# Performance work log

Measured on AMD Instinct MI355X. Metric: run time of the kernel, lower is better.

Reference implementation:

```python
import jax, jax.numpy as jnp
import numpy as np

K = 5        # kernel_size per pseudo-dim
DIM = 2      # pseudo-coordinate dimensionality
K2 = K * K   # total kernel weight matrices
N_NODES = 50000


def spline_basis(edge_attr):
    """Open B-spline basis, degree=1, dim=2. Returns basis [E,4], weight_index [E,4]."""
    v = edge_attr * (K - 1)                      # [E,2], pseudo in [0,1]
    lo = jnp.floor(v)
    frac = v - lo                                # [E,2]
    lo = lo.astype(jnp.int32)
    fac = jnp.stack([1.0 - frac, frac], axis=-1)                 # [E,2,2] (dim, bit)
    idx = jnp.clip(lo[..., None] + jnp.arange(2), 0, K - 1)      # [E,2,2]
    b0 = jnp.array([0, 1, 0, 1])  # bit for dim 0, per spline term
    b1 = jnp.array([0, 0, 1, 1])  # bit for dim 1
    basis = fac[:, 0, b0] * fac[:, 1, b1]        # [E,4]
    wi = idx[:, 0, b0] * K + idx[:, 1, b1]       # [E,4] flat kernel index
    return basis, wi


def spline_conv(x, src, dst, basis, wi, W, root, bias, n_nodes):
    """SplineConv with mean aggregation, root weight and bias.
    x:[N,Fin] W:[K2,Fin,Fout] root:[Fin,Fout] bias:[Fout]"""
    E = src.shape[0]
    K2_, Fin, Fout = W.shape
    # scatter the 4 sparse basis values into a dense per-edge kernel-coeff matrix [E,K2]
    coeff = jnp.zeros((E, K2_), x.dtype).at[jnp.arange(E)[:, None], wi].add(basis)
    xj = x[src]                                  # gather source features [E,Fin]
    msg = jnp.zeros((E, Fout), x.dtype)
    for k in range(K2_):                         # fixed small loop over 25 kernels
        msg = msg + coeff[:, k:k + 1] * (xj @ W[k])
    agg = jax.ops.segment_sum(msg, dst, num_segments=n_nodes)    # [N,Fout]
    deg = jax.ops.segment_sum(jnp.ones((E,), x.dtype), dst, num_segments=n_nodes)
    agg = agg / jnp.clip(deg, 1.0)[:, None]      # mean aggregation
    return agg + x @ root + bias


def setup_inputs() -> dict:
    key = jax.random.key(0)
    ks = jax.random.split(key, 9)
    E = 800000
    Fin, H, C = 64, 16, 7
    x = jax.random.normal(ks[0], (N_NODES, Fin), dtype=jnp.float32)
    edge_index = jax.random.randint(ks[1], (2, E), 0, N_NODES, dtype=jnp.int64)
    edge_attr = jax.random.uniform(ks[2], (E, DIM), dtype=jnp.float32)
    s1 = 1.0 / np.sqrt(Fin)
    s2 = 1.0 / np.sqrt(H)
    W1 = jax.random.uniform(ks[3], (K2, Fin, H), jnp.float32, -s1, s1)
    root1 = jax.random.uniform(ks[4], (Fin, H), jnp.float32, -s1, s1)
    bias1 = jax.random.uniform(ks[5], (H,), jnp.float32, -s1, s1)
    W2 = jax.random.uniform(ks[6], (K2, H, C), jnp.float32, -s2, s2)
    root2 = jax.random.uniform(ks[7], (H, C), jnp.float32, -s2, s2)
    bias2 = jax.random.uniform(ks[8], (C,), jnp.float32, -s2, s2)
    return {"x": x, "edge_index": edge_index, "edge_attr": edge_attr,
            "W1": W1, "root1": root1, "bias1": bias1,
            "W2": W2, "root2": root2, "bias2": bias2}


def reference(x, edge_index, edge_attr, W1, root1, bias1, W2, root2, bias2):
    src = edge_index[0]
    dst = edge_index[1]
    basis, wi = spline_basis(edge_attr)
    h = jax.nn.relu(spline_conv(x, src, dst, basis, wi, W1, root1, bias1, N_NODES))
    # dropout(p=0.6) is identity in eval mode
    out = spline_conv(h, src, dst, basis, wi, W2, root2, bias2, N_NODES)
    return jax.nn.log_softmax(out, axis=1)
```

## Files before the change

### kernel.cpp

```cpp
#include <hip/hip_runtime.h>

#define KK2 25
#define FIN 64
#define HH 16
#define CC 7

#define SCAN_VPT 4
#define SCAN_BLK 256
#define SCAN_CHUNK (SCAN_VPT * SCAN_BLK)

__global__ void k_hist(const int* __restrict__ ei, int* __restrict__ cnt, int E) {
    int e = blockIdx.x * 256 + threadIdx.x;
    if (e < E) atomicAdd(&cnt[ei[E + e]], 1);
}

__global__ void k_bsum(const int* __restrict__ cnt, int* __restrict__ bsum, int N) {
    int b = blockIdx.x, t = threadIdx.x;
    int base = b * SCAN_CHUNK + t * SCAN_VPT;
    int s = 0;
#pragma unroll
    for (int j = 0; j < SCAN_VPT; j++) {
        int i = base + j;
        if (i < N) s += cnt[i];
    }
#pragma unroll
    for (int d = 1; d < 64; d <<= 1) s += __shfl_xor(s, d, 64);
    __shared__ int sd[SCAN_BLK / 64];
    if ((t & 63) == 0) sd[t >> 6] = s;
    __syncthreads();
    if (t == 0) {
        int tot = 0;
        for (int w = 0; w < SCAN_BLK / 64; w++) tot += sd[w];
        bsum[b] = tot;
    }
}

__global__ void k_bscan(const int* __restrict__ bsum, int* __restrict__ boff, int nblk) {
    int t = threadIdx.x;
    __shared__ int sd[256];
    int v = (t < nblk) ? bsum[t] : 0;
    sd[t] = v;
    __syncthreads();
    for (int off = 1; off < 256; off <<= 1) {
        int u = (t >= off) ? sd[t - off] : 0;
        __syncthreads();
        sd[t] += u;
        __syncthreads();
    }
    boff[t] = sd[t] - v;
}

__global__ void k_sfin(const int* __restrict__ cnt, const int* __restrict__ boff,
                       int* __restrict__ rowStart, int* __restrict__ cursor, int N) {
    int b = blockIdx.x, t = threadIdx.x;
    int base = b * SCAN_CHUNK + t * SCAN_VPT;
    int v[SCAN_VPT];
    int s = 0;
#pragma unroll
    for (int j = 0; j < SCAN_VPT; j++) {
        int i = base + j;
        v[j] = (i < N) ? cnt[i] : 0;
        s += v[j];
    }
    __shared__ int sd[SCAN_BLK];
    sd[t] = s;
    __syncthreads();
    for (int off = 1; off < SCAN_BLK; off <<= 1) {
        int u = (t >= off) ? sd[t - off] : 0;
        __syncthreads();
        sd[t] += u;
        __syncthreads();
    }
    int run = sd[t] - s + boff[b];
#pragma unroll
    for (int j = 0; j < SCAN_VPT; j++) {
        int i = base + j;
        if (i < N) {
            rowStart[i] = run;
            cursor[i] = run;
            run += v[j];
            if (i == N - 1) rowStart[N] = run;
        }
    }
}

__global__ void k_scatter(const float* __restrict__ attr, const int* __restrict__ ei,
                          int* __restrict__ cursor, float4* __restrict__ rec, int E) {
    int e = blockIdx.x * 256 + threadIdx.x;
    if (e >= E) return;
    float v0 = attr[2 * e] * 4.0f, v1 = attr[2 * e + 1] * 4.0f;
    float l0 = floorf(v0), l1 = floorf(v1);
    float f0 = v0 - l0, f1 = v1 - l1;
    int i0 = (int)l0, i1 = (int)l1;
    int i0a = min(max(i0, 0), 4), i0b = min(max(i0 + 1, 0), 4);
    int i1a = min(max(i1, 0), 4), i1b = min(max(i1 + 1, 0), 4);
    float4 b;
    b.x = (1.0f - f0) * (1.0f - f1);
    b.y = f0 * (1.0f - f1);
    b.z = (1.0f - f0) * f1;
    b.w = f0 * f1;
    unsigned pack = (unsigned)(i0a * 5 + i1a) | ((unsigned)(i0b * 5 + i1a) << 8) |
                    ((unsigned)(i0a * 5 + i1b) << 16) | ((unsigned)(i0b * 5 + i1b) << 24);
    int s = ei[e], d = ei[E + e];
    int pos = atomicAdd(&cursor[d], 1);
    rec[2 * pos] = b;
    rec[2 * pos + 1] = make_float4(__int_as_float(s), __uint_as_float(pack), 0.0f, 0.0f);
}

__global__ void k_prepW(const float* __restrict__ W1, const float* __restrict__ W2,
                        float* __restrict__ B1t, float* __restrict__ W2p) {
    int tid = blockIdx.x * 256 + threadIdx.x;
    if (tid < KK2 * FIN * HH) {
        int c = tid >> 6, i = tid & 63;
        int k = c >> 4, h = c & 15;
        B1t[tid] = W1[(k * FIN + i) * HH + h];
    }
    if (tid < KK2 * HH * CC) {
        int k = tid / (HH * CC), r = tid % (HH * CC);
        int i = r / CC, c = r % CC;
        W2p[(k * HH + i) * 8 + c] = W2[tid];
    }
}

__global__ void k_y1(const float* __restrict__ x, const float* __restrict__ B1t,
                     float* __restrict__ y1, int N, int nb) {
    int g = blockIdx.x / nb;
    int n = (blockIdx.x % nb) * 256 + threadIdx.x;
    if (n >= N) return;
    float4 xr[16];
    const float4* xp = (const float4*)(x + (size_t)n * 64);
#pragma unroll
    for (int i = 0; i < 16; i++) xr[i] = xp[i];
    const float* B = B1t + g * 80 * 64;
    float4 acc[20];
#pragma unroll
    for (int cg = 0; cg < 20; cg++) {
        float a0 = 0, a1 = 0, a2 = 0, a3 = 0;
        const float4* b0 = (const float4*)(B + (cg * 4 + 0) * 64);
        const float4* b1 = (const float4*)(B + (cg * 4 + 1) * 64);
        const float4* b2 = (const float4*)(B + (cg * 4 + 2) * 64);
        const float4* b3 = (const float4*)(B + (cg * 4 + 3) * 64);
#pragma unroll
        for (int i = 0; i < 16; i++) {
            float4 xi = xr[i];
            float4 v0 = b0[i], v1 = b1[i], v2 = b2[i], v3 = b3[i];
            a0 += xi.x * v0.x + xi.y * v0.y + xi.z * v0.z + xi.w * v0.w;
            a1 += xi.x * v1.x + xi.y * v1.y + xi.z * v1.z + xi.w * v1.w;
            a2 += xi.x * v2.x + xi.y * v2.y + xi.z * v2.z + xi.w * v2.w;
            a3 += xi.x * v3.x + xi.y * v3.y + xi.z * v3.z + xi.w * v3.w;
        }
        acc[cg] = make_float4(a0, a1, a2, a3);
    }
    float4* yo = (float4*)(y1 + (size_t)n * 400 + g * 80);
#pragma unroll
    for (int cg = 0; cg < 20; cg++) yo[cg] = acc[cg];
}

__global__ void k_agg1(const int* __restrict__ rowStart, const float4* __restrict__ rec,
                       const float* __restrict__ y1, float* __restrict__ agg1, int N) {
    int n = blockIdx.x * 4 + (threadIdx.x >> 6);
    if (n >= N) return;
    int lane = threadIdx.x & 63;
    int sub = lane >> 4, h = lane & 15;
    int start = rowStart[n], end = rowStart[n + 1];
    float acc = 0.0f;
    for (int i = start + sub; i < end; i += 4) {
        float4 b = rec[2 * i];
        float4 meta = rec[2 * i + 1];
        int s = __float_as_int(meta.x);
        unsigned w = __float_as_uint(meta.y);
        const float* yr = y1 + (size_t)s * 400;
        acc += b.x * yr[(w & 255u) * 16 + h];
        acc += b.y * yr[((w >> 8) & 255u) * 16 + h];
        acc += b.z * yr[((w >> 16) & 255u) * 16 + h];
        acc += b.w * yr[(w >> 24) * 16 + h];
    }
    acc += __shfl_xor(acc, 16, 64);
    acc += __shfl_xor(acc, 32, 64);
    if (lane < 16) agg1[(size_t)n * 16 + h] = acc;
}

__global__ void k_upd1(const float* __restrict__ x, const float* __restrict__ agg1,
                       const int* __restrict__ rowStart, const float* __restrict__ root1,
                       const float* __restrict__ bias1, float* __restrict__ h1, int N) {
    int n = blockIdx.x * 256 + threadIdx.x;
    if (n >= N) return;
    float inv = 1.0f / (float)max(rowStart[n + 1] - rowStart[n], 1);
    float r[16];
#pragma unroll
    for (int h = 0; h < 16; h++) r[h] = agg1[(size_t)n * 16 + h] * inv + bias1[h];
    const float* xrow = x + (size_t)n * 64;
    for (int i = 0; i < 64; i++) {
        float xi = xrow[i];
        const float* rr = root1 + i * 16;
#pragma unroll
        for (int h = 0; h < 16; h++) r[h] += xi * rr[h];
    }
    float* ho = h1 + (size_t)n * 16;
#pragma unroll
    for (int h = 0; h < 16; h++) ho[h] = fmaxf(r[h], 0.0f);
}

__global__ void k_y2(const float* __restrict__ h1, const float* __restrict__ W2p,
                     float* __restrict__ y2, int N) {
    int n = blockIdx.x * 256 + threadIdx.x;
    if (n >= N) return;
    float h[16];
    const float4* hp = (const float4*)(h1 + (size_t)n * 16);
#pragma unroll
    for (int j = 0; j < 4; j++) {
        float4 v = hp[j];
        h[4 * j] = v.x; h[4 * j + 1] = v.y; h[4 * j + 2] = v.z; h[4 * j + 3] = v.w;
    }
    float4* yo = (float4*)(y2 + (size_t)n * 200);
    for (int k = 0; k < 25; k++) {
        float4 zlo = make_float4(0, 0, 0, 0), zhi = make_float4(0, 0, 0, 0);
        const float4* wp = (const float4*)(W2p + k * 128);
#pragma unroll
        for (int i = 0; i < 16; i++) {
            float hi = h[i];
            float4 lo = wp[2 * i], hv = wp[2 * i + 1];
            zlo.x += hi * lo.x; zlo.y += hi * lo.y; zlo.z += hi * lo.z; zlo.w += hi * lo.w;
            zhi.x += hi * hv.x; zhi.y += hi * hv.y; zhi.z += hi * hv.z; zhi.w += hi * hv.w;
        }
        yo[2 * k] = zlo;
        yo[2 * k + 1] = zhi;
    }
}

__global__ void k_agg2(const int* __restrict__ rowStart, const float4* __restrict__ rec,
                       const float* __restrict__ y2, float* __restrict__ agg2, int N) {
    int n = blockIdx.x * 4 + (threadIdx.x >> 6);
    if (n >= N) return;
    int lane = threadIdx.x & 63;
    int sub = lane >> 3, c = lane & 7;
    int start = rowStart[n], end = rowStart[n + 1];
    float acc = 0.0f;
    for (int i = start + sub; i < end; i += 8) {
        float4 b = rec[2 * i];
        float4 meta = rec[2 * i + 1];
        int s = __float_as_int(meta.x);
        unsigned w = __float_as_uint(meta.y);
        const float* yr = y2 + (size_t)s * 200;
        acc += b.x * yr[(w & 255u) * 8 + c];
        acc += b.y * yr[((w >> 8) & 255u) * 8 + c];
        acc += b.z * yr[((w >> 16) & 255u) * 8 + c];
        acc += b.w * yr[(w >> 24) * 8 + c];
    }
    acc += __shfl_xor(acc, 8, 64);
    acc += __shfl_xor(acc, 16, 64);
    acc += __shfl_xor(acc, 32, 64);
    if (lane < 8) agg2[(size_t)n * 8 + c] = acc;
}

__global__ void k_fin2(const float* __restrict__ h1, const float* __restrict__ agg2,
                       const int* __restrict__ rowStart, const float* __restrict__ root2,
                       const float* __restrict__ bias2, float* __restrict__ out, int N) {
    int n = blockIdx.x * 256 + threadIdx.x;
    if (n >= N) return;
    float inv = 1.0f / (float)max(rowStart[n + 1] - rowStart[n], 1);
    float z[7];
#pragma unroll
    for (int c = 0; c < 7; c++) z[c] = agg2[(size_t)n * 8 + c] * inv + bias2[c];
    const float* hrow = h1 + (size_t)n * 16;
#pragma unroll
    for (int i = 0; i < 16; i++) {
        float hi = hrow[i];
        const float* rr = root2 + i * 7;
#pragma unroll
        for (int c = 0; c < 7; c++) z[c] += hi * rr[c];
    }
    float m = z[0];
#pragma unroll
    for (int c = 1; c < 7; c++) m = fmaxf(m, z[c]);
    float ssum = 0.0f;
#pragma unroll
    for (int c = 0; c < 7; c++) ssum += expf(z[c] - m);
    float ls = logf(ssum);
    float* orow = out + (size_t)n * 7;
#pragma unroll
    for (int c = 0; c < 7; c++) orow[c] = z[c] - m - ls;
}

extern "C" void kernel_launch(void* const* d_in, const int* in_sizes, int n_in,
                              void* d_out, int out_size, void* d_ws, size_t ws_size,
                              hipStream_t stream) {
    const float* x     = (const float*)d_in[0];
    const int*   ei    = (const int*)d_in[1];
    const float* attr  = (const float*)d_in[2];
    const float* W1    = (const float*)d_in[3];
    const float* root1 = (const float*)d_in[4];
    const float* bias1 = (const float*)d_in[5];
    const float* W2    = (const float*)d_in[6];
    const float* root2 = (const float*)d_in[7];
    const float* bias2 = (const float*)d_in[8];
    float* out = (float*)d_out;

    int N = in_sizes[0] / FIN;
    int E = in_sizes[1] / 2;

    char* w = (char*)d_ws;
    size_t off = 0;
    auto alloc = [&](size_t bytes) -> void* {
        void* p = w + off;
        off += (bytes + 255) & ~(size_t)255;
        return p;
    };
    int*      cnt      = (int*)alloc((size_t)N * 4);
    int*      rowStart = (int*)alloc((size_t)(N + 1) * 4);
    int*      cursor   = (int*)alloc((size_t)N * 4);
    int*      bsum     = (int*)alloc(260 * 4);
    int*      boff     = (int*)alloc(260 * 4);
    float4*   rec      = (float4*)alloc((size_t)E * 32);
    float*    agg1     = (float*)alloc((size_t)N * 64);
    float*    h1       = (float*)alloc((size_t)N * 64);
    float*    agg2     = (float*)alloc((size_t)N * 32);
    float*    B1t      = (float*)alloc((size_t)KK2 * FIN * HH * 4);
    float*    W2p      = (float*)alloc((size_t)KK2 * HH * 8 * 4);
    float*    y1       = (float*)alloc((size_t)N * 400 * 4);
    float*    y2       = y1;
    (void)ws_size; (void)n_in; (void)out_size;

    hipMemsetAsync(cnt, 0, (size_t)N * 4, stream);

    int ebl = (E + 255) / 256;
    int nbl = (N + 255) / 256;
    int sblk = (N + SCAN_CHUNK - 1) / SCAN_CHUNK;

    k_hist<<<ebl, 256, 0, stream>>>(ei, cnt, E);
    k_bsum<<<sblk, SCAN_BLK, 0, stream>>>(cnt, bsum, N);
    k_bscan<<<1, 256, 0, stream>>>(bsum, boff, sblk);
    k_sfin<<<sblk, SCAN_BLK, 0, stream>>>(cnt, boff, rowStart, cursor, N);
    k_scatter<<<ebl, 256, 0, stream>>>(attr, ei, cursor, rec, E);
    k_prepW<<<(KK2 * FIN * HH + 255) / 256, 256, 0, stream>>>(W1, W2, B1t, W2p);
    k_y1<<<5 * nbl, 256, 0, stream>>>(x, B1t, y1, N, nbl);
    k_agg1<<<(N + 3) / 4, 256, 0, stream>>>(rowStart, rec, y1, agg1, N);
    k_upd1<<<nbl, 256, 0, stream>>>(x, agg1, rowStart, root1, bias1, h1, N);
    k_y2<<<nbl, 256, 0, stream>>>(h1, W2p, y2, N);
    k_agg2<<<(N + 3) / 4, 256, 0, stream>>>(rowStart, rec, y2, agg2, N);
    k_fin2<<<nbl, 256, 0, stream>>>(h1, agg2, rowStart, root2, bias2, out, N);
}
```

Baseline: 343.8 us.

## Transpose y1/y2 to kernel-major layout, fuse y2 into update, single-pass y1

Stores the per-node precomputed products y1 and y2 in [k][node][feature] order instead of [node][k][feature]. Each thread in k_y1 now loops over all 25 kernels, which reduces the grid from five times as many blocks to one per node group. The y2 computation is fused into k_upd1, so h1 no longer has to be re-read. Write coalescing changes: a thread's 16 floats for one k are now contiguous and adjacent threads write adjacent rows. Gathers in the aggregation kernels become scattered across far-apart k planes rather than within one 1.6KB node row, which may hurt cache locality, and the single-block-per-node y1 kernel has fewer waves in flight.

```diff
diff --git a/kernel.cpp b/kernel.cpp
--- a/kernel.cpp
+++ b/kernel.cpp
@@ -123,57 +123,58 @@
 }
 
 __global__ void k_y1(const float* __restrict__ x, const float* __restrict__ B1t,
-                     float* __restrict__ y1, int N, int nb) {
-    int g = blockIdx.x / nb;
-    int n = (blockIdx.x % nb) * 256 + threadIdx.x;
+                     float* __restrict__ y1T, int N) {
+    int n = blockIdx.x * 256 + threadIdx.x;
     if (n >= N) return;
     float4 xr[16];
     const float4* xp = (const float4*)(x + (size_t)n * 64);
 #pragma unroll
     for (int i = 0; i < 16; i++) xr[i] = xp[i];
-    const float* B = B1t + g * 80 * 64;
-    float4 acc[20];
-#pragma unroll
-    for (int cg = 0; cg < 20; cg++) {
-        float a0 = 0, a1 = 0, a2 = 0, a3 = 0;
-        const float4* b0 = (const float4*)(B + (cg * 4 + 0) * 64);
-        const float4* b1 = (const float4*)(B + (cg * 4 + 1) * 64);
-        const float4* b2 = (const float4*)(B + (cg * 4 + 2) * 64);
-        const float4* b3 = (const float4*)(B + (cg * 4 + 3) * 64);
-#pragma unroll
-        for (int i = 0; i < 16; i++) {
-            float4 xi = xr[i];
-            float4 v0 = b0[i], v1 = b1[i], v2 = b2[i], v3 = b3[i];
-            a0 += xi.x * v0.x + xi.y * v0.y + xi.z * v0.z + xi.w * v0.w;
-            a1 += xi.x * v1.x + xi.y * v1.y + xi.z * v1.z + xi.w * v1.w;
-            a2 += xi.x * v2.x + xi.y * v2.y + xi.z * v2.z + xi.w * v2.w;
-            a3 += xi.x * v3.x + xi.y * v3.y + xi.z * v3.z + xi.w * v3.w;
+    for (int k = 0; k < 25; k++) {
+        const float* B = B1t + k * 16 * 64;
+        float4 acc[4];
+#pragma unroll
+        for (int h4 = 0; h4 < 4; h4++) {
+            float a0 = 0, a1 = 0, a2 = 0, a3 = 0;
+            const float4* b0 = (const float4*)(B + (h4 * 4 + 0) * 64);
+            const float4* b1 = (const float4*)(B + (h4 * 4 + 1) * 64);
+            const float4* b2 = (const float4*)(B + (h4 * 4 + 2) * 64);
+            const float4* b3 = (const float4*)(B + (h4 * 4 + 3) * 64);
+#pragma unroll
+            for (int i = 0; i < 16; i++) {
+                float4 xi = xr[i];
+                float4 v0 = b0[i], v1 = b1[i], v2 = b2[i], v3 = b3[i];
+                a0 += xi.x * v0.x + xi.y * v0.y + xi.z * v0.z + xi.w * v0.w;
+                a1 += xi.x * v1.x + xi.y * v1.y + xi.z * v1.z + xi.w * v1.w;
+                a2 += xi.x * v2.x + xi.y * v2.y + xi.z * v2.z + xi.w * v2.w;
+                a3 += xi.x * v3.x + xi.y * v3.y + xi.z * v3.z + xi.w * v3.w;
+            }
+            acc[h4] = make_float4(a0, a1, a2, a3);
         }
-        acc[cg] = make_float4(a0, a1, a2, a3);
-    }
-    float4* yo = (float4*)(y1 + (size_t)n * 400 + g * 80);
-#pragma unroll
-    for (int cg = 0; cg < 20; cg++) yo[cg] = acc[cg];
+        float4* yo = (float4*)(y1T + ((size_t)k * N + n) * 16);
+#pragma unroll
+        for (int h4 = 0; h4 < 4; h4++) yo[h4] = acc[h4];
+    }
 }
 
 __global__ void k_agg1(const int* __restrict__ rowStart, const float4* __restrict__ rec,
-                       const float* __restrict__ y1, float* __restrict__ agg1, int N) {
+                       const float* __restrict__ y1T, float* __restrict__ agg1, int N) {
     int n = blockIdx.x * 4 + (threadIdx.x >> 6);
     if (n >= N) return;
     int lane = threadIdx.x & 63;
     int sub = lane >> 4, h = lane & 15;
     int start = rowStart[n], end = rowStart[n + 1];
     float acc = 0.0f;
+    size_t NN = (size_t)N;
     for (int i = start + sub; i < end; i += 4) {
         float4 b = rec[2 * i];
         float4 meta = rec[2 * i + 1];
         int s = __float_as_int(meta.x);
         unsigned w = __float_as_uint(meta.y);
-        const float* yr = y1 + (size_t)s * 400;
-        acc += b.x * yr[(w & 255u) * 16 + h];
-        acc += b.y * yr[((w >> 8) & 255u) * 16 + h];
-        acc += b.z * yr[((w >> 16) & 255u) * 16 + h];
-        acc += b.w * yr[(w >> 24) * 16 + h];
+        acc += b.x * y1T[((w & 255u) * NN + s) * 16 + h];
+        acc += b.y * y1T[(((w >> 8) & 255u) * NN + s) * 16 + h];
+        acc += b.z * y1T[(((w >> 16) & 255u) * NN + s) * 16 + h];
+        acc += b.w * y1T[((w >> 24) * NN + s) * 16 + h];
     }
     acc += __shfl_xor(acc, 16, 64);
     acc += __shfl_xor(acc, 32, 64);
@@ -182,7 +183,8 @@
 
 __global__ void k_upd1(const float* __restrict__ x, const float* __restrict__ agg1,
                        const int* __restrict__ rowStart, const float* __restrict__ root1,
-                       const float* __restrict__ bias1, float* __restrict__ h1, int N) {
+                       const float* __restrict__ bias1, const float* __restrict__ W2p,
+                       float* __restrict__ h1, float* __restrict__ y2T, int N) {
     int n = blockIdx.x * 256 + threadIdx.x;
     if (n >= N) return;
     float inv = 1.0f / (float)max(rowStart[n + 1] - rowStart[n], 1);
@@ -196,56 +198,45 @@
 #pragma unroll
         for (int h = 0; h < 16; h++) r[h] += xi * rr[h];
     }
-    float* ho = h1 + (size_t)n * 16;
-#pragma unroll
-    for (int h = 0; h < 16; h++) ho[h] = fmaxf(r[h], 0.0f);
-}
-
-__global__ void k_y2(const float* __restrict__ h1, const float* __restrict__ W2p,
-                     float* __restrict__ y2, int N) {
-    int n = blockIdx.x * 256 + threadIdx.x;
-    if (n >= N) return;
-    float h[16];
-    const float4* hp = (const float4*)(h1 + (size_t)n * 16);
-#pragma unroll
-    for (int j = 0; j < 4; j++) {
-        float4 v = hp[j];
-        h[4 * j] = v.x; h[4 * j + 1] = v.y; h[4 * j + 2] = v.z; h[4 * j + 3] = v.w;
-    }
-    float4* yo = (float4*)(y2 + (size_t)n * 200);
+#pragma unroll
+    for (int h = 0; h < 16; h++) r[h] = fmaxf(r[h], 0.0f);
+    float4* ho = (float4*)(h1 + (size_t)n * 16);
+#pragma unroll
+    for (int j = 0; j < 4; j++) ho[j] = make_float4(r[4*j], r[4*j+1], r[4*j+2], r[4*j+3]);
     for (int k = 0; k < 25; k++) {
         float4 zlo = make_float4(0, 0, 0, 0), zhi = make_float4(0, 0, 0, 0);
         const float4* wp = (const float4*)(W2p + k * 128);
 #pragma unroll
         for (int i = 0; i < 16; i++) {
-            float hi = h[i];
+            float hi = r[i];
             float4 lo = wp[2 * i], hv = wp[2 * i + 1];
             zlo.x += hi * lo.x; zlo.y += hi * lo.y; zlo.z += hi * lo.z; zlo.w += hi * lo.w;
             zhi.x += hi * hv.x; zhi.y += hi * hv.y; zhi.z += hi * hv.z; zhi.w += hi * hv.w;
         }
-        yo[2 * k] = zlo;
-        yo[2 * k + 1] = zhi;
+        float4* yo = (float4*)(y2T + ((size_t)k * N + n) * 8);
+        yo[0] = zlo;
+        yo[1] = zhi;
     }
 }
 
 __global__ void k_agg2(const int* __restrict__ rowStart, const float4* __restrict__ rec,
-                       const float* __restrict__ y2, float* __restrict__ agg2, int N) {
+                       const float* __restrict__ y2T, float* __restrict__ agg2, int N) {
     int n = blockIdx.x * 4 + (threadIdx.x >> 6);
     if (n >= N) return;
     int lane = threadIdx.x & 63;
     int sub = lane >> 3, c = lane & 7;
     int start = rowStart[n], end = rowStart[n + 1];
     float acc = 0.0f;
+    size_t NN = (size_t)N;
     for (int i = start + sub; i < end; i += 8) {
         float4 b = rec[2 * i];
         float4 meta = rec[2 * i + 1];
         int s = __float_as_int(meta.x);
         unsigned w = __float_as_uint(meta.y);
-        const float* yr = y2 + (size_t)s * 200;
-        acc += b.x * yr[(w & 255u) * 8 + c];
-        acc += b.y * yr[((w >> 8) & 255u) * 8 + c];
-        acc += b.z * yr[((w >> 16) & 255u) * 8 + c];
-        acc += b.w * yr[(w >> 24) * 8 + c];
+        acc += b.x * y2T[((w & 255u) * NN + s) * 8 + c];
+        acc += b.y * y2T[(((w >> 8) & 255u) * NN + s) * 8 + c];
+        acc += b.z * y2T[(((w >> 16) & 255u) * NN + s) * 8 + c];
+        acc += b.w * y2T[((w >> 24) * NN + s) * 8 + c];
     }
     acc += __shfl_xor(acc, 8, 64);
     acc += __shfl_xor(acc, 16, 64);
@@ -317,8 +308,8 @@
     float*    agg2     = (float*)alloc((size_t)N * 32);
     float*    B1t      = (float*)alloc((size_t)KK2 * FIN * HH * 4);
     float*    W2p      = (float*)alloc((size_t)KK2 * HH * 8 * 4);
-    float*    y1       = (float*)alloc((size_t)N * 400 * 4);
-    float*    y2       = y1;
+    float*    y1T      = (float*)alloc((size_t)N * 400 * 4);
+    float*    y2T      = y1T;
     (void)ws_size; (void)n_in; (void)out_size;
 
     hipMemsetAsync(cnt, 0, (size_t)N * 4, stream);
@@ -333,10 +324,9 @@
     k_sfin<<<sblk, SCAN_BLK, 0, stream>>>(cnt, boff, rowStart, cursor, N);
     k_scatter<<<ebl, 256, 0, stream>>>(attr, ei, cursor, rec, E);
     k_prepW<<<(KK2 * FIN * HH + 255) / 256, 256, 0, stream>>>(W1, W2, B1t, W2p);
-    k_y1<<<5 * nbl, 256, 0, stream>>>(x, B1t, y1, N, nbl);
-    k_agg1<<<(N + 3) / 4, 256, 0, stream>>>(rowStart, rec, y1, agg1, N);
-    k_upd1<<<nbl, 256, 0, stream>>>(x, agg1, rowStart, root1, bias1, h1, N);
-    k_y2<<<nbl, 256, 0, stream>>>(h1, W2p, y2, N);
-    k_agg2<<<(N + 3) / 4, 256, 0, stream>>>(rowStart, rec, y2, agg2, N);
+    k_y1<<<nbl, 256, 0, stream>>>(x, B1t, y1T, N);
+    k_agg1<<<(N + 3) / 4, 256, 0, stream>>>(rowStart, rec, y1T, agg1, N);
+    k_upd1<<<nbl, 256, 0, stream>>>(x, agg1, rowStart, root1, bias1, W2p, h1, y2T, N);
+    k_agg2<<<(N + 3) / 4, 256, 0, stream>>>(rowStart, rec, y2T, agg2, N);
     k_fin2<<<nbl, 256, 0, stream>>>(h1, agg2, rowStart, root2, bias2, out, N);
 }
```

After: 494.4 us. +43.8%, slower.
